# Performance work log

Hardware: AMD Instinct MI355X
Metric: run time of the kernel (lower is better)

The kernel has to match this reference:

```python
import jax, jax.numpy as jnp
import numpy as np

K = 7            # filter_size
N_ITERS = 5
SXY_G = 3.0      # gaussian spatial sigma
SRGB = 10.0      # bilateral color sigma
COMPAT_G = 3.0
COMPAT_B = 10.0


def _gaussian_kernel(size, sigma):
    coords = jnp.arange(size, dtype=jnp.float32) - (size - 1) / 2.0
    g = jnp.exp(-coords ** 2 / (2.0 * sigma ** 2))
    g = g / g.sum()
    return g[None, :] * g[:, None]  # (K, K), row-major flatten matches torch view


def _unfold(x, k):
    # x: (B,C,H,W) -> (B,C,k*k,H,W), zero padding, patch elements in row-major
    # order (ki*k + kj), matching F.unfold + view(B,C,k*k,H,W).
    B, C, H, W = x.shape
    p = k // 2
    xp = jnp.pad(x, ((0, 0), (0, 0), (p, p), (p, p)))
    patches = [xp[:, :, i:i + H, j:j + W] for i in range(k) for j in range(k)]
    return jnp.stack(patches, axis=2)


def setup_inputs() -> dict:
    key = jax.random.key(0)
    k1, k2 = jax.random.split(key)
    B, C, H, W = 2, 29, 256, 256
    unary = jax.random.normal(k1, (B, C, H, W), dtype=jnp.float32)
    img = jax.random.uniform(k2, (B, 3, H, W), dtype=jnp.float32) * 255.0  # RGB [0,255]
    return {"unary": unary, "img": img}


def reference(unary, img):
    # unary: (B,C,H,W) logits (neg log prob); img: (B,3,H,W)
    spatial = _gaussian_kernel(K, SXY_G).reshape(-1)        # (K*K,)
    sw = spatial[None, None, :, None, None]                 # (1,1,K2,1,1)

    # Precompute bilateral weights once (as in the torch module)
    img_unfold = _unfold(img, K)                            # (B,3,K2,H,W)
    diff_sq = ((img_unfold - img[:, :, None]) ** 2).sum(axis=1, keepdims=True)
    bilateral = jnp.exp(-diff_sq / (2.0 * SRGB ** 2)) * sw  # (B,1,K2,H,W)

    q = jax.nn.softmax(-unary, axis=1)
    for _ in range(N_ITERS):
        q_unf = _unfold(q, K)                   # (B,C,K2,H,W)
        msg_b = (q_unf * bilateral).sum(axis=2) # bilateral message
        # depthwise gaussian conv with zero padding == gaussian-weighted patch sum
        msg_g = (q_unf * sw).sum(axis=2)
        pairwise = COMPAT_G * msg_g + COMPAT_B * msg_b
        q = jax.nn.softmax(-unary + pairwise, axis=1)
    return q
```

## Files before the change

### kernel.cpp

```cpp
#include <hip/hip_runtime.h>
#include <hip/hip_fp16.h>

#define CNUM 29
#define HH 256
#define WW 256
#define BB 2
#define KK 7
#define HALO 3
#define TX 32
#define TY 4
#define LW (TX + 2*HALO)
#define LH (TY + 2*HALO)
#define NPIX (LH*LW)
#define HWP (HH*WW)

__device__ constexpr float GW[KK] = {
    0.106287146f, 0.140321912f, 0.165770643f, 0.175240699f,
    0.165770643f, 0.140321912f, 0.106287146f};

__device__ __forceinline__ unsigned packh2(float a, float b) {
    __half2 h = __floats2half2_rn(a, b);
    return *reinterpret_cast<unsigned*>(&h);
}
__device__ __forceinline__ float2 unpkh2(unsigned u) {
    __half2 h = *reinterpret_cast<__half2*>(&u);
    return __half22float2(h);
}

template <bool FIRST, bool LAST>
__global__ __launch_bounds__(256) void crf_iter(const float* __restrict__ unary,
                                                const float* __restrict__ img,
                                                const uint4* __restrict__ qin,
                                                uint4* __restrict__ qout,
                                                uint4* __restrict__ uh,
                                                float* __restrict__ outf) {
    __shared__ uint4 s_q4[NPIX * 4];
    __shared__ float s_im[3][NPIX];

    const int tid = threadIdx.x;
    const bool isA = tid < 128;
    const int lid = tid & 127;
    const int tx = lid & (TX - 1);
    const int ty = lid >> 5;
    const int bx = blockIdx.x * TX;
    const int by = blockIdx.y * TY;
    const int b  = blockIdx.z;

    const float* ubase = unary + (size_t)b * CNUM * HWP;
    const float* imgb  = img + (size_t)b * 3 * HWP;

    for (int t = tid; t < NPIX; t += 256) {
        int r = t / LW, cc = t - r * LW;
        int gy = by + r - HALO, gx = bx + cc - HALO;
        bool ok = (gy >= 0) & (gy < HH) & (gx >= 0) & (gx < WW);
        int goff = ok ? gy * WW + gx : 0;
        float i0 = imgb[goff], i1 = imgb[HWP + goff], i2 = imgb[2 * HWP + goff];
        if (!ok) { i0 = 0.f; i1 = 0.f; i2 = 0.f; }
        s_im[0][t] = i0; s_im[1][t] = i1; s_im[2][t] = i2;

        const int swz = (t >> 1) & 3;
        if (FIRST) {
            float nu[CNUM];
            float mm = -1e30f;
#pragma unroll
            for (int c = 0; c < CNUM; ++c) {
                nu[c] = -ubase[(size_t)c * HWP + goff];
                mm = fmaxf(mm, nu[c]);
            }
            bool interior = (r >= HALO) & (r < LH - HALO) & (cc >= HALO) & (cc < LW - HALO);
            if (interior) {
                uint4* up = uh + ((size_t)b * HWP + goff) * 4;
                uint4 u0, u1, u2, u3;
                u0.x = packh2(nu[0],  nu[1]);  u0.y = packh2(nu[2],  nu[3]);
                u0.z = packh2(nu[4],  nu[5]);  u0.w = packh2(nu[6],  nu[7]);
                u1.x = packh2(nu[8],  nu[9]);  u1.y = packh2(nu[10], nu[11]);
                u1.z = packh2(nu[12], nu[13]); u1.w = packh2(nu[14], nu[15]);
                u2.x = packh2(nu[16], nu[17]); u2.y = packh2(nu[18], nu[19]);
                u2.z = packh2(nu[20], nu[21]); u2.w = packh2(nu[22], nu[23]);
                u3.x = packh2(nu[24], nu[25]); u3.y = packh2(nu[26], nu[27]);
                u3.z = packh2(nu[28], 0.f);    u3.w = 0u;
                up[0] = u0; up[1] = u1; up[2] = u2; up[3] = u3;
            }
            float ss = 0.f;
            float v[CNUM];
#pragma unroll
            for (int c = 0; c < CNUM; ++c) { v[c] = __expf(nu[c] - mm); ss += v[c]; }
            float inv = ok ? 1.f / ss : 0.f;
#pragma unroll
            for (int c = 0; c < CNUM; ++c) v[c] *= inv;
            uint4 p0, p1, p2, p3;
            p0.x = packh2(v[0],  v[1]);  p0.y = packh2(v[2],  v[3]);
            p0.z = packh2(v[4],  v[5]);  p0.w = packh2(v[6],  v[7]);
            p1.x = packh2(v[8],  v[9]);  p1.y = packh2(v[10], v[11]);
            p1.z = packh2(v[12], v[13]); p1.w = packh2(v[14], v[15]);
            p2.x = packh2(v[16], v[17]); p2.y = packh2(v[18], v[19]);
            p2.z = packh2(v[20], v[21]); p2.w = packh2(v[22], v[23]);
            p3.x = packh2(v[24], v[25]); p3.y = packh2(v[26], v[27]);
            p3.z = packh2(v[28], 0.f);   p3.w = 0u;
            s_q4[t * 4 + (0 ^ swz)] = p0;
            s_q4[t * 4 + (1 ^ swz)] = p1;
            s_q4[t * 4 + (2 ^ swz)] = p2;
            s_q4[t * 4 + (3 ^ swz)] = p3;
        } else {
            const uint4* qp = qin + ((size_t)b * HWP + goff) * 4;
            uint4 p0 = qp[0], p1 = qp[1], p2 = qp[2], p3 = qp[3];
            if (!ok) {
                p0.x = p0.y = p0.z = p0.w = 0u;
                p1.x = p1.y = p1.z = p1.w = 0u;
                p2.x = p2.y = p2.z = p2.w = 0u;
                p3.x = p3.y = p3.z = p3.w = 0u;
            }
            s_q4[t * 4 + (0 ^ swz)] = p0;
            s_q4[t * 4 + (1 ^ swz)] = p1;
            s_q4[t * 4 + (2 ^ swz)] = p2;
            s_q4[t * 4 + (3 ^ swz)] = p3;
        }
    }
    __syncthreads();

    const int tc = (ty + HALO) * LW + (tx + HALO);
    const float c0 = s_im[0][tc];
    const float c1 = s_im[1][tc];
    const float c2 = s_im[2][tc];

    float acc[CNUM];
#pragma unroll
    for (int c = 0; c < CNUM; ++c) acc[c] = 0.f;

#define TAP_BODY(ii)                                                        \
    {                                                                       \
        const int t = (ty + (ii)) * LW + (tx + j);                          \
        float d0 = s_im[0][t] - c0;                                         \
        float d1 = s_im[1][t] - c1;                                         \
        float d2 = s_im[2][t] - c2;                                         \
        float dsq = d0 * d0 + d1 * d1 + d2 * d2;                            \
        float w = (GW[(ii)] * GW[j]) * (3.0f + 10.0f * __expf(dsq * -0.005f)); \
        const int t4 = t * 4;                                               \
        const int swz = (t >> 1) & 3;                                       \
        uint4 q0 = s_q4[t4 + (0 ^ swz)];                                    \
        uint4 q1 = s_q4[t4 + (1 ^ swz)];                                    \
        uint4 q2 = s_q4[t4 + (2 ^ swz)];                                    \
        uint4 q3 = s_q4[t4 + (3 ^ swz)];                                    \
        const unsigned* u0 = &q0.x;                                         \
        const unsigned* u1 = &q1.x;                                         \
        const unsigned* u2 = &q2.x;                                         \
        _Pragma("unroll")                                                   \
        for (int k = 0; k < 4; ++k) {                                       \
            float2 f = unpkh2(u0[k]);                                       \
            acc[2 * k]     += w * f.x;                                      \
            acc[2 * k + 1] += w * f.y;                                      \
        }                                                                   \
        _Pragma("unroll")                                                   \
        for (int k = 0; k < 4; ++k) {                                       \
            float2 f = unpkh2(u1[k]);                                       \
            acc[8 + 2 * k]     += w * f.x;                                  \
            acc[8 + 2 * k + 1] += w * f.y;                                  \
        }                                                                   \
        _Pragma("unroll")                                                   \
        for (int k = 0; k < 4; ++k) {                                       \
            float2 f = unpkh2(u2[k]);                                       \
            acc[16 + 2 * k]     += w * f.x;                                 \
            acc[16 + 2 * k + 1] += w * f.y;                                 \
        }                                                                   \
        {                                                                   \
            float2 f = unpkh2(q3.x);                                        \
            acc[24] += w * f.x; acc[25] += w * f.y;                         \
            f = unpkh2(q3.y);                                               \
            acc[26] += w * f.x; acc[27] += w * f.y;                         \
            f = unpkh2(q3.z);                                               \
            acc[28] += w * f.x;                                             \
        }                                                                   \
    }

    if (isA) {
#pragma unroll
        for (int i = 0; i < 4; ++i)
#pragma unroll
            for (int j = 0; j < KK; ++j) TAP_BODY(i)
    } else {
#pragma unroll
        for (int i = 4; i < KK; ++i)
#pragma unroll
            for (int j = 0; j < KK; ++j) TAP_BODY(i)
    }
#undef TAP_BODY

    __syncthreads();
    float* s_part = reinterpret_cast<float*>(s_q4);
    if (!isA) {
#pragma unroll
        for (int c = 0; c < CNUM; ++c) s_part[c * 128 + lid] = acc[c];
    }
    __syncthreads();

    if (isA) {
        const int pix = (by + ty) * WW + (bx + tx);
        float l[CNUM];
        if (FIRST) {
#pragma unroll
            for (int c = 0; c < CNUM; ++c)
                l[c] = acc[c] + s_part[c * 128 + lid] - ubase[(size_t)c * HWP + pix];
        } else {
            const uint4* up = uh + ((size_t)b * HWP + pix) * 4;
            uint4 n0 = up[0], n1 = up[1], n2 = up[2], n3 = up[3];
            const unsigned* w0 = &n0.x;
            const unsigned* w1 = &n1.x;
            const unsigned* w2 = &n2.x;
            float nu[CNUM];
#pragma unroll
            for (int k = 0; k < 4; ++k) {
                float2 f = unpkh2(w0[k]); nu[2 * k] = f.x; nu[2 * k + 1] = f.y;
            }
#pragma unroll
            for (int k = 0; k < 4; ++k) {
                float2 f = unpkh2(w1[k]); nu[8 + 2 * k] = f.x; nu[8 + 2 * k + 1] = f.y;
            }
#pragma unroll
            for (int k = 0; k < 4; ++k) {
                float2 f = unpkh2(w2[k]); nu[16 + 2 * k] = f.x; nu[16 + 2 * k + 1] = f.y;
            }
            { float2 f = unpkh2(n3.x); nu[24] = f.x; nu[25] = f.y; }
            { float2 f = unpkh2(n3.y); nu[26] = f.x; nu[27] = f.y; }
            { float2 f = unpkh2(n3.z); nu[28] = f.x; }
#pragma unroll
            for (int c = 0; c < CNUM; ++c)
                l[c] = acc[c] + s_part[c * 128 + lid] + nu[c];
        }
        float m = l[0];
#pragma unroll
        for (int c = 1; c < CNUM; ++c) m = fmaxf(m, l[c]);
        float ss = 0.f;
#pragma unroll
        for (int c = 0; c < CNUM; ++c) { l[c] = __expf(l[c] - m); ss += l[c]; }
        float inv = 1.0f / ss;

        if (LAST) {
            float* qo = outf + (size_t)b * CNUM * HWP + pix;
#pragma unroll
            for (int c = 0; c < CNUM; ++c) qo[(size_t)c * HWP] = l[c] * inv;
        } else {
            uint4 p0, p1, p2, p3;
            p0.x = packh2(l[0] * inv,  l[1] * inv);
            p0.y = packh2(l[2] * inv,  l[3] * inv);
            p0.z = packh2(l[4] * inv,  l[5] * inv);
            p0.w = packh2(l[6] * inv,  l[7] * inv);
            p1.x = packh2(l[8] * inv,  l[9] * inv);
            p1.y = packh2(l[10] * inv, l[11] * inv);
            p1.z = packh2(l[12] * inv, l[13] * inv);
            p1.w = packh2(l[14] * inv, l[15] * inv);
            p2.x = packh2(l[16] * inv, l[17] * inv);
            p2.y = packh2(l[18] * inv, l[19] * inv);
            p2.z = packh2(l[20] * inv, l[21] * inv);
            p2.w = packh2(l[22] * inv, l[23] * inv);
            p3.x = packh2(l[24] * inv, l[25] * inv);
            p3.y = packh2(l[26] * inv, l[27] * inv);
            p3.z = packh2(l[28] * inv, 0.f);
            p3.w = 0u;
            uint4* qo = qout + ((size_t)b * HWP + pix) * 4;
            qo[0] = p0; qo[1] = p1; qo[2] = p2; qo[3] = p3;
        }
    }
}

extern "C" void kernel_launch(void* const* d_in, const int* in_sizes, int n_in,
                              void* d_out, int out_size, void* d_ws, size_t ws_size,
                              hipStream_t stream) {
    const float* unary = (const float*)d_in[0];
    const float* img   = (const float*)d_in[1];
    const size_t QBYTES = (size_t)BB * HWP * 64;
    uint4* qA = (uint4*)d_ws;
    uint4* qB = (uint4*)((char*)d_ws + QBYTES);
    uint4* uh = (uint4*)((char*)d_ws + 2 * QBYTES);
    float* outf = (float*)d_out;

    dim3 grid(WW / TX, HH / TY, BB);
    crf_iter<true,  false><<<grid, 256, 0, stream>>>(unary, img, qB, qA, uh, outf);
    crf_iter<false, false><<<grid, 256, 0, stream>>>(unary, img, qA, qB, uh, outf);
    crf_iter<false, false><<<grid, 256, 0, stream>>>(unary, img, qB, qA, uh, outf);
    crf_iter<false, false><<<grid, 256, 0, stream>>>(unary, img, qA, qB, uh, outf);
    crf_iter<false, true ><<<grid, 256, 0, stream>>>(unary, img, qB, qA, uh, outf);
}
```

Before: 100.0 us.

## Swizzle block order, pack image in LDS, and issue halo loads together

Remaps the flat block index so consecutive workgroups are spread across tiles, which is likely intended to improve cache or XCD locality. The RGB values in LDS are stored as a float2 plus a float, so each tap needs two shared loads instead of three. For non-first iterations the halo-load loop is unrolled into two explicit loads issued before any stores, which raises memory-level parallelism. The row split between the two thread halves is also swapped so the 3-row group does the final epilogue work, which may balance load better.

Measured after the change: 93.70 us. 1.07x faster.

```diff
diff --git a/kernel.cpp b/kernel.cpp
--- a/kernel.cpp
+++ b/kernel.cpp
@@ -34,32 +34,38 @@
                                                 uint4* __restrict__ qout,
                                                 uint4* __restrict__ uh,
                                                 float* __restrict__ outf) {
-    __shared__ uint4 s_q4[NPIX * 4];
-    __shared__ float s_im[3][NPIX];
+    __shared__ uint4  s_q4[NPIX * 4];
+    __shared__ float2 s_im2[NPIX];
+    __shared__ float  s_imz[NPIX];
 
     const int tid = threadIdx.x;
     const bool isA = tid < 128;
     const int lid = tid & 127;
     const int tx = lid & (TX - 1);
     const int ty = lid >> 5;
-    const int bx = blockIdx.x * TX;
-    const int by = blockIdx.y * TY;
-    const int b  = blockIdx.z;
+
+    const int flat = (blockIdx.z << 9) | (blockIdx.y << 3) | blockIdx.x;
+    const int sid  = ((flat & 7) << 7) | (flat >> 3);
+    const int b    = sid >> 9;
+    const int rem  = sid & 511;
+    const int by   = (rem >> 3) * TY;
+    const int bx   = (rem & 7) * TX;
+    const int pix  = (by + ty) * WW + (bx + tx);
 
     const float* ubase = unary + (size_t)b * CNUM * HWP;
     const float* imgb  = img + (size_t)b * 3 * HWP;
 
-    for (int t = tid; t < NPIX; t += 256) {
-        int r = t / LW, cc = t - r * LW;
-        int gy = by + r - HALO, gx = bx + cc - HALO;
-        bool ok = (gy >= 0) & (gy < HH) & (gx >= 0) & (gx < WW);
-        int goff = ok ? gy * WW + gx : 0;
-        float i0 = imgb[goff], i1 = imgb[HWP + goff], i2 = imgb[2 * HWP + goff];
-        if (!ok) { i0 = 0.f; i1 = 0.f; i2 = 0.f; }
-        s_im[0][t] = i0; s_im[1][t] = i1; s_im[2][t] = i2;
-
-        const int swz = (t >> 1) & 3;
-        if (FIRST) {
+    if (FIRST) {
+        for (int t = tid; t < NPIX; t += 256) {
+            int r = t / LW, cc = t - r * LW;
+            int gy = by + r - HALO, gx = bx + cc - HALO;
+            bool ok = (gy >= 0) & (gy < HH) & (gx >= 0) & (gx < WW);
+            int goff = ok ? gy * WW + gx : 0;
+            float i0 = imgb[goff], i1 = imgb[HWP + goff], i2 = imgb[2 * HWP + goff];
+            if (!ok) { i0 = 0.f; i1 = 0.f; i2 = 0.f; }
+            float2 v2; v2.x = i0; v2.y = i1;
+            s_im2[t] = v2; s_imz[t] = i2;
+
             float nu[CNUM];
             float mm = -1e30f;
 #pragma unroll
@@ -88,6 +94,7 @@
             float inv = ok ? 1.f / ss : 0.f;
 #pragma unroll
             for (int c = 0; c < CNUM; ++c) v[c] *= inv;
+            const int swz = (t >> 1) & 3;
             uint4 p0, p1, p2, p3;
             p0.x = packh2(v[0],  v[1]);  p0.y = packh2(v[2],  v[3]);
             p0.z = packh2(v[4],  v[5]);  p0.w = packh2(v[6],  v[7]);
@@ -101,27 +108,64 @@
             s_q4[t * 4 + (1 ^ swz)] = p1;
             s_q4[t * 4 + (2 ^ swz)] = p2;
             s_q4[t * 4 + (3 ^ swz)] = p3;
-        } else {
-            const uint4* qp = qin + ((size_t)b * HWP + goff) * 4;
-            uint4 p0 = qp[0], p1 = qp[1], p2 = qp[2], p3 = qp[3];
-            if (!ok) {
-                p0.x = p0.y = p0.z = p0.w = 0u;
-                p1.x = p1.y = p1.z = p1.w = 0u;
-                p2.x = p2.y = p2.z = p2.w = 0u;
-                p3.x = p3.y = p3.z = p3.w = 0u;
-            }
-            s_q4[t * 4 + (0 ^ swz)] = p0;
-            s_q4[t * 4 + (1 ^ swz)] = p1;
-            s_q4[t * 4 + (2 ^ swz)] = p2;
-            s_q4[t * 4 + (3 ^ swz)] = p3;
+        }
+    } else {
+        int t = tid;
+        int r = t / LW, cc = t - r * LW;
+        int gy = by + r - HALO, gx = bx + cc - HALO;
+        bool ok = (gy >= 0) & (gy < HH) & (gx >= 0) & (gx < WW);
+        int goff = ok ? gy * WW + gx : 0;
+        float i0 = imgb[goff], i1 = imgb[HWP + goff], i2 = imgb[2 * HWP + goff];
+        const uint4* qp = qin + ((size_t)b * HWP + goff) * 4;
+        uint4 p0 = qp[0], p1 = qp[1], p2 = qp[2], p3 = qp[3];
+
+        int t2 = tid + 256;
+        bool has2 = t2 < NPIX;
+        int r2 = t2 / LW, cc2 = t2 - r2 * LW;
+        int gy2 = by + r2 - HALO, gx2 = bx + cc2 - HALO;
+        bool ok2 = has2 & (gy2 >= 0) & (gy2 < HH) & (gx2 >= 0) & (gx2 < WW);
+        int goff2 = ok2 ? gy2 * WW + gx2 : 0;
+        float j0 = 0.f, j1 = 0.f, j2 = 0.f;
+        uint4 s0, s1, s2, s3;
+        if (has2) {
+            j0 = imgb[goff2]; j1 = imgb[HWP + goff2]; j2 = imgb[2 * HWP + goff2];
+            const uint4* qp2 = qin + ((size_t)b * HWP + goff2) * 4;
+            s0 = qp2[0]; s1 = qp2[1]; s2 = qp2[2]; s3 = qp2[3];
+        }
+        if (!ok) {
+            i0 = 0.f; i1 = 0.f; i2 = 0.f;
+            p0.x = p0.y = p0.z = p0.w = 0u; p1.x = p1.y = p1.z = p1.w = 0u;
+            p2.x = p2.y = p2.z = p2.w = 0u; p3.x = p3.y = p3.z = p3.w = 0u;
+        }
+        float2 v2; v2.x = i0; v2.y = i1;
+        s_im2[t] = v2; s_imz[t] = i2;
+        const int swz = (t >> 1) & 3;
+        s_q4[t * 4 + (0 ^ swz)] = p0;
+        s_q4[t * 4 + (1 ^ swz)] = p1;
+        s_q4[t * 4 + (2 ^ swz)] = p2;
+        s_q4[t * 4 + (3 ^ swz)] = p3;
+        if (has2) {
+            if (!ok2) {
+                j0 = 0.f; j1 = 0.f; j2 = 0.f;
+                s0.x = s0.y = s0.z = s0.w = 0u; s1.x = s1.y = s1.z = s1.w = 0u;
+                s2.x = s2.y = s2.z = s2.w = 0u; s3.x = s3.y = s3.z = s3.w = 0u;
+            }
+            float2 w2; w2.x = j0; w2.y = j1;
+            s_im2[t2] = w2; s_imz[t2] = j2;
+            const int swz2 = (t2 >> 1) & 3;
+            s_q4[t2 * 4 + (0 ^ swz2)] = s0;
+            s_q4[t2 * 4 + (1 ^ swz2)] = s1;
+            s_q4[t2 * 4 + (2 ^ swz2)] = s2;
+            s_q4[t2 * 4 + (3 ^ swz2)] = s3;
         }
     }
     __syncthreads();
 
     const int tc = (ty + HALO) * LW + (tx + HALO);
-    const float c0 = s_im[0][tc];
-    const float c1 = s_im[1][tc];
-    const float c2 = s_im[2][tc];
+    const float2 cv = s_im2[tc];
+    const float c0 = cv.x;
+    const float c1 = cv.y;
+    const float c2 = s_imz[tc];
 
     float acc[CNUM];
 #pragma unroll
@@ -130,9 +174,10 @@
 #define TAP_BODY(ii)                                                        \
     {                                                                       \
         const int t = (ty + (ii)) * LW + (tx + j);                          \
-        float d0 = s_im[0][t] - c0;                                         \
-        float d1 = s_im[1][t] - c1;                                         \
-        float d2 = s_im[2][t] - c2;                                         \
+        float2 iv = s_im2[t];                                               \
+        float d0 = iv.x - c0;                                               \
+        float d1 = iv.y - c1;                                               \
+        float d2 = s_imz[t] - c2;                                           \
         float dsq = d0 * d0 + d1 * d1 + d2 * d2;                            \
         float w = (GW[(ii)] * GW[j]) * (3.0f + 10.0f * __expf(dsq * -0.005f)); \
         const int t4 = t * 4;                                               \
@@ -174,12 +219,12 @@
 
     if (isA) {
 #pragma unroll
-        for (int i = 0; i < 4; ++i)
+        for (int i = 4; i < KK; ++i)
 #pragma unroll
             for (int j = 0; j < KK; ++j) TAP_BODY(i)
     } else {
 #pragma unroll
-        for (int i = 4; i < KK; ++i)
+        for (int i = 0; i < 4; ++i)
 #pragma unroll
             for (int j = 0; j < KK; ++j) TAP_BODY(i)
     }
@@ -194,7 +239,6 @@
     __syncthreads();
 
     if (isA) {
-        const int pix = (by + ty) * WW + (bx + tx);
         float l[CNUM];
         if (FIRST) {
 #pragma unroll
```
